# Performance work log

Measured on AMD Instinct MI355X. Metric: run time of the kernel, lower is better.

The kernel has to match this reference:

```python
import jax, jax.numpy as jnp
import numpy as np

B_SZ, L, D_MODEL = 4, 4096, 512
D_INNER, N_HEADS, HEAD_DIM = 1024, 16, 64
D_STATE, D_CONV, CHUNK = 64, 4, 64
EPS = 1e-5


def setup_inputs() -> dict:
    key = jax.random.key(0)
    ks = jax.random.split(key, 12)
    return {
        'x': jax.random.normal(ks[0], (B_SZ, L, D_MODEL), jnp.float32),
        'W_in': jax.random.normal(ks[1], (D_MODEL, 2 * D_INNER), jnp.float32) * 0.02,
        'conv_x_kernel': jax.random.normal(ks[2], (D_CONV, 1, D_INNER), jnp.float32) * 0.1,
        'conv_x_bias': jnp.zeros((D_INNER,), jnp.float32),
        'conv_z_kernel': jax.random.normal(ks[3], (D_CONV, 1, D_INNER), jnp.float32) * 0.1,
        'conv_z_bias': jnp.zeros((D_INNER,), jnp.float32),
        'W_xdbl': jax.random.normal(ks[4], (D_INNER, N_HEADS + 2 * D_STATE), jnp.float32) * 0.02,
        'dt_bias': jax.random.normal(ks[5], (N_HEADS,), jnp.float32) * 0.5,
        'A_log': jax.random.uniform(ks[6], (N_HEADS,), jnp.float32, 0.0, 1.0),
        'D': jnp.ones((N_HEADS,), jnp.float32),
        'norm_weight': jnp.ones((D_INNER,), jnp.float32),
        'W_out': jax.random.normal(ks[7], (D_INNER, D_MODEL), jnp.float32) * 0.02,
    }


def dwconv(x, kernel, bias):
    # x: (b, l, d); kernel: (k, 1, d) depthwise, flax 'SAME' padding
    out = jax.lax.conv_general_dilated(
        x, kernel, window_strides=(1,), padding='SAME',
        dimension_numbers=('NWC', 'WIO', 'NWC'),
        feature_group_count=x.shape[-1])
    return out + bias


def segsum(a):
    # stable segment-sum: out[..., d, e] = sum_{e < i <= d} a[..., i]; -inf above diag
    T = a.shape[-1]
    a_rep = jnp.broadcast_to(a[..., :, None], a.shape + (T,))
    strict = jnp.tril(jnp.ones((T, T), bool), -1)
    seg = jnp.cumsum(jnp.where(strict, a_rep, 0.0), axis=-2)
    return jnp.where(jnp.tril(jnp.ones((T, T), bool)), seg, -jnp.inf)


def ssd(x, A, B, C, chunk):
    # x: (b,l,h,p), A: (b,l,h), B/C: (b,l,n) (single group, broadcast over heads)
    b, l, h, p = x.shape
    c = l // chunk
    x = x.reshape(b, c, chunk, h, p)
    A = A.reshape(b, c, chunk, h).transpose(0, 3, 1, 2)  # (b,h,c,l)
    B = B.reshape(b, c, chunk, -1)
    C = C.reshape(b, c, chunk, -1)
    A_cum = jnp.cumsum(A, axis=-1)
    Lmat = jnp.exp(segsum(A))  # (b,h,c,l,l)
    Y_diag = jnp.einsum('bcln,bcsn,bhcls,bcshp->bclhp', C, B, Lmat, x)
    decay_states = jnp.exp(A_cum[..., -1:] - A_cum)
    states = jnp.einsum('bcln,bhcl,bclhp->bchpn', B, decay_states, x)
    states = jnp.concatenate([jnp.zeros_like(states[:, :1]), states], axis=1)
    A_last = jnp.pad(A_cum[..., -1], ((0, 0), (0, 0), (1, 0)))
    decay_chunk = jnp.exp(segsum(A_last))  # (b,h,c+1,c+1)
    new_states = jnp.einsum('bhzc,bchpn->bzhpn', decay_chunk, states)
    states, final_state = new_states[:, :-1], new_states[:, -1]
    Y_off = jnp.einsum('bcln,bchpn,bhcl->bclhp', C, states, jnp.exp(A_cum))
    Y = (Y_diag + Y_off).reshape(b, l, h, p)
    return Y, final_state


def reference(x, W_in, conv_x_kernel, conv_x_bias, conv_z_kernel, conv_z_bias,
              W_xdbl, dt_bias, A_log, D, norm_weight, W_out):
    b, l, _ = x.shape
    xz = x @ W_in
    xi, z = jnp.split(xz, 2, axis=-1)
    xi = jax.nn.silu(dwconv(xi, conv_x_kernel, conv_x_bias))
    z = jax.nn.silu(dwconv(z, conv_z_kernel, conv_z_bias))
    x_dbl = xi @ W_xdbl  # (b,l,h+2n)
    dt = x_dbl[..., :N_HEADS]
    Bmat = x_dbl[..., N_HEADS:N_HEADS + D_STATE]
    Cmat = x_dbl[..., N_HEADS + D_STATE:]
    dt = jax.nn.softplus(dt + dt_bias)  # (b,l,h)
    A = -jnp.exp(A_log)  # (h,)
    xh = xi.reshape(b, l, N_HEADS, HEAD_DIM)
    y, _ = ssd(xh * dt[..., None], A * dt, Bmat, Cmat, CHUNK)
    y = y + xh * D[..., None]
    y = y.reshape(b, l, D_INNER)
    # gated RMSNorm (Mamba2 style): gate with silu(z), then rmsnorm with weight
    y = y * jax.nn.silu(z)
    y = y * jax.lax.rsqrt(jnp.mean(y * y, axis=-1, keepdims=True) + EPS) * norm_weight
    return y @ W_out
```

## Files before the change

kernel.cpp:

```cpp
#include <hip/hip_runtime.h>
#include <hip/hip_bf16.h>
#include <cstdint>

#define B_SZn 4
#define SEQ_L 4096
#define D_MODELn 512
#define D_INNERn 1024
#define N_HEADSn 16
#define HEAD_DIMn 64
#define D_STATEn 64
#define CHUNKn 64
#define NCHUNK (SEQ_L / CHUNKn)
#define BL (B_SZn * SEQ_L)
#define XDBL_N (N_HEADSn + 2 * D_STATEn)

typedef __hip_bfloat16 bf16;
typedef __bf16 bf16x8 __attribute__((ext_vector_type(8)));
typedef float f32x4 __attribute__((ext_vector_type(4)));

__device__ __forceinline__ float silu_f(float v) {
    return v / (1.0f + expf(-v));
}
__device__ __forceinline__ float b2f(unsigned short u) {
    return __uint_as_float((unsigned)u << 16);
}
__device__ __forceinline__ unsigned short f2b(float f) {
    bf16 h = __float2bfloat16(f);
    return *(unsigned short*)&h;
}
__device__ __forceinline__ void stf(float* p, float v) { *p = v; }
__device__ __forceinline__ void stf(bf16* p, float v) { *p = __float2bfloat16(v); }

__device__ __forceinline__ float4 us4_to_f4(ushort4 u) {
    float4 f;
    f.x = b2f(u.x); f.y = b2f(u.y); f.z = b2f(u.z); f.w = b2f(u.w);
    return f;
}

__device__ __forceinline__ void async_copy16(void* lds, const void* g) {
    __builtin_amdgcn_global_load_lds(
        (const __attribute__((address_space(1))) unsigned int*)g,
        (__attribute__((address_space(3))) unsigned int*)lds, 16, 0, 0);
}

__global__ __launch_bounds__(256) void cvt_f32_bf16(
    const float* __restrict__ in, bf16* __restrict__ out) {
    const int idx = blockIdx.x * 256 + threadIdx.x;
    float4 v = *(const float4*)(in + (size_t)idx * 4);
    ushort4 o;
    o.x = f2b(v.x); o.y = f2b(v.y); o.z = f2b(v.z); o.w = f2b(v.w);
    *(ushort4*)((unsigned short*)out + (size_t)idx * 4) = o;
}

__global__ __launch_bounds__(256) void transpose_cvt(
    const float* __restrict__ in, bf16* __restrict__ out, int R, int C) {
    __shared__ float t[32][33];
    const int bc = blockIdx.x * 32, br = blockIdx.y * 32;
    const int tx = threadIdx.x & 31, ty = threadIdx.x >> 5;
#pragma unroll
    for (int i = ty; i < 32; i += 8) {
        int r = br + i, c = bc + tx;
        t[i][tx] = (r < R && c < C) ? in[(size_t)r * C + c] : 0.f;
    }
    __syncthreads();
#pragma unroll
    for (int i = ty; i < 32; i += 8) {
        int c = bc + i, r = br + tx;
        if (c < C && r < R) out[(size_t)c * R + r] = __float2bfloat16(t[tx][i]);
    }
}

template <typename TO>
__global__ __launch_bounds__(256) void gemm_mfma(
    const bf16* __restrict__ A, const bf16* __restrict__ Bt,
    TO* __restrict__ C, int M, int N, int K) {
    __shared__ __align__(16) unsigned short Al[2][128 * 32];
    __shared__ __align__(16) unsigned short Bl[2][128 * 32];
    const int tid = threadIdx.x;
    const int wave = tid >> 6, lane = tid & 63;
    const int wm = (wave >> 1) * 64, wn = (wave & 1) * 64;
    int lin = blockIdx.y * gridDim.x + blockIdx.x;
    const int nwg = gridDim.x * gridDim.y;
    if ((nwg & 7) == 0) lin = (lin & 7) * (nwg >> 3) + (lin >> 3);
    const int bm = (lin / gridDim.x) * 128, bn = (lin % gridDim.x) * 128;
    f32x4 acc[4][4];
#pragma unroll
    for (int m = 0; m < 4; ++m)
#pragma unroll
        for (int n = 0; n < 4; ++n) acc[m][n] = (f32x4)(0.f);

    const int lrow = lane & 15, lk8 = (lane >> 4) * 8;
    const int srow = tid >> 2, sc8 = (tid & 3) * 8;
    for (int k0 = 0; k0 < K; k0 += 64) {
#pragma unroll
        for (int h = 0; h < 2; ++h) {
            const int kh = k0 + h * 32;
            async_copy16((char*)&Al[h][0] + (size_t)(wave * 64) * 16,
                         A + (size_t)(bm + srow) * K + kh + sc8);
            async_copy16((char*)&Al[h][0] + (size_t)(256 + wave * 64) * 16,
                         A + (size_t)(bm + 64 + srow) * K + kh + sc8);
            async_copy16((char*)&Bl[h][0] + (size_t)(wave * 64) * 16,
                         Bt + (size_t)(bn + srow) * K + kh + sc8);
            async_copy16((char*)&Bl[h][0] + (size_t)(256 + wave * 64) * 16,
                         Bt + (size_t)(bn + 64 + srow) * K + kh + sc8);
        }
        __syncthreads();
#pragma unroll
        for (int h = 0; h < 2; ++h) {
            bf16x8 af[4], bfr[4];
#pragma unroll
            for (int m = 0; m < 4; ++m)
                af[m] = *(const bf16x8*)(&Al[h][(wm + m * 16 + lrow) * 32 + lk8]);
#pragma unroll
            for (int n = 0; n < 4; ++n)
                bfr[n] = *(const bf16x8*)(&Bl[h][(wn + n * 16 + lrow) * 32 + lk8]);
#pragma unroll
            for (int m = 0; m < 4; ++m)
#pragma unroll
                for (int n = 0; n < 4; ++n)
                    acc[m][n] = __builtin_amdgcn_mfma_f32_16x16x32_bf16(
                        af[m], bfr[n], acc[m][n], 0, 0, 0);
        }
        __syncthreads();
    }
#pragma unroll
    for (int m = 0; m < 4; ++m) {
#pragma unroll
        for (int n = 0; n < 4; ++n) {
#pragma unroll
            for (int r = 0; r < 4; ++r) {
                int row = bm + wm + m * 16 + (lane >> 4) * 4 + r;
                int col = bn + wn + n * 16 + (lane & 15);
                if (row < M && col < N)
                    stf(&C[(size_t)row * N + col], acc[m][n][r]);
            }
        }
    }
}

__global__ __launch_bounds__(256) void conv_silu_kernel(
    const bf16* __restrict__ xz,
    const float* __restrict__ kx, const float* __restrict__ bx,
    const float* __restrict__ kz, const float* __restrict__ bz,
    bf16* __restrict__ xi, bf16* __restrict__ zo) {
    const int tid = threadIdx.x;
    const int d4 = tid * 4;
    const int blk = blockIdx.x;
    const int l0 = (blk * 8) & (SEQ_L - 1);
    const int b = (blk * 8) >> 12;
    const unsigned short* base = (const unsigned short*)xz +
                                 ((size_t)b * SEQ_L) * (2 * D_INNERn);
    float4 wx[4], wz[4];
#pragma unroll
    for (int k = 0; k < 4; ++k) {
        wx[k] = *(const float4*)(kx + k * D_INNERn + d4);
        wz[k] = *(const float4*)(kz + k * D_INNERn + d4);
    }
    const float4 bxv = *(const float4*)(bx + d4);
    const float4 bzv = *(const float4*)(bz + d4);
    float4 vx[4], vz[4];
#pragma unroll
    for (int j = 0; j < 3; ++j) {
        int l = l0 - 1 + j;
        if (l >= 0) {
            const unsigned short* row = base + (size_t)l * (2 * D_INNERn);
            vx[j] = us4_to_f4(*(const ushort4*)(row + d4));
            vz[j] = us4_to_f4(*(const ushort4*)(row + D_INNERn + d4));
        } else {
            vx[j] = make_float4(0.f, 0.f, 0.f, 0.f);
            vz[j] = make_float4(0.f, 0.f, 0.f, 0.f);
        }
    }
    unsigned short* xout = (unsigned short*)xi;
    unsigned short* zout = (unsigned short*)zo;
#pragma unroll
    for (int j = 0; j < 8; ++j) {
        const int lread = l0 + 2 + j;
        if (lread < SEQ_L) {
            const unsigned short* row = base + (size_t)lread * (2 * D_INNERn);
            vx[3] = us4_to_f4(*(const ushort4*)(row + d4));
            vz[3] = us4_to_f4(*(const ushort4*)(row + D_INNERn + d4));
        } else {
            vx[3] = make_float4(0.f, 0.f, 0.f, 0.f);
            vz[3] = make_float4(0.f, 0.f, 0.f, 0.f);
        }
        float4 ax = bxv, az = bzv;
#pragma unroll
        for (int k = 0; k < 4; ++k) {
            ax.x += vx[k].x * wx[k].x; ax.y += vx[k].y * wx[k].y;
            ax.z += vx[k].z * wx[k].z; ax.w += vx[k].w * wx[k].w;
            az.x += vz[k].x * wz[k].x; az.y += vz[k].y * wz[k].y;
            az.z += vz[k].z * wz[k].z; az.w += vz[k].w * wz[k].w;
        }
        ushort4 ox, oz;
        ox.x = f2b(silu_f(ax.x)); ox.y = f2b(silu_f(ax.y));
        ox.z = f2b(silu_f(ax.z)); ox.w = f2b(silu_f(ax.w));
        oz.x = f2b(silu_f(az.x)); oz.y = f2b(silu_f(az.y));
        oz.z = f2b(silu_f(az.z)); oz.w = f2b(silu_f(az.w));
        const size_t obase = ((size_t)b * SEQ_L + l0 + j) * D_INNERn + d4;
        *(ushort4*)(xout + obase) = ox;
        *(ushort4*)(zout + obase) = oz;
        vx[0] = vx[1]; vx[1] = vx[2]; vx[2] = vx[3];
        vz[0] = vz[1]; vz[1] = vz[2]; vz[2] = vz[3];
    }
}

__global__ __launch_bounds__(256) void dt_kernel(
    const unsigned short* __restrict__ xdbl, const float* __restrict__ dt_bias,
    float* __restrict__ dtp) {
    const int idx = blockIdx.x * 256 + threadIdx.x;
    const int h = idx & 15;
    const int r = idx >> 4;
    float v = b2f(xdbl[(size_t)r * XDBL_N + h]) + dt_bias[h];
    dtp[idx] = (v > 20.f) ? v : log1pf(expf(v));
}

__global__ __launch_bounds__(256) void ssd_chunk_mfma(
    const unsigned short* __restrict__ xdbl, const bf16* __restrict__ xi,
    const float* __restrict__ dtp, const float* __restrict__ A_log,
    const float* __restrict__ Dvec,
    unsigned short* __restrict__ y, unsigned short* __restrict__ S,
    float* __restrict__ acum_g, float* __restrict__ rchunk) {
    __shared__ __align__(16) unsigned short sBb[64 * 72];
    __shared__ __align__(16) unsigned short sCb[64 * 72];
    __shared__ __align__(16) unsigned short sXT[64 * 72];
    __shared__ __align__(16) unsigned short sGb[64 * 72];
    __shared__ __align__(16) unsigned short sWB[64 * 72];
    __shared__ float sdtp[64], sacum[64], sw[64];
    const int bid = blockIdx.x;
    const int h = bid & 15;
    const int bc = bid >> 4;
    const int c = bc & (NCHUNK - 1);
    const int b = bc >> 6;
    const int tid = threadIdx.x;
    const int wave = tid >> 6, lane = tid & 63;
    const int lrow = lane & 15, lk8 = (lane >> 4) * 8;
    const int row0 = b * SEQ_L + c * CHUNKn;
    const float Ah = -expf(A_log[h]);
    const float Dh = Dvec[h];

    if (tid < 64) sdtp[tid] = dtp[(size_t)(row0 + tid) * N_HEADSn + h];
    const unsigned short* xius = (const unsigned short*)xi;
#pragma unroll
    for (int it = 0; it < 16; ++it) {
        int e = tid + it * 256;
        int s = e >> 6, n = e & 63;
        const unsigned short* xr = xdbl + (size_t)(row0 + s) * XDBL_N + N_HEADSn;
        sBb[s * 72 + n] = xr[n];
        sCb[s * 72 + n] = xr[D_STATEn + n];
        sXT[n * 72 + s] = xius[(size_t)(row0 + s) * D_INNERn + h * HEAD_DIMn + n];
    }
    __syncthreads();
    if (wave == 0) {
        float v = Ah * sdtp[lane];
#pragma unroll
        for (int o = 1; o < 64; o <<= 1) {
            float t = __shfl_up(v, o);
            if (lane >= o) v += t;
        }
        sacum[lane] = v;
        float last = __shfl(v, 63);
        sw[lane] = expf(last - v) * sdtp[lane];
        acum_g[(size_t)bid * 64 + lane] = v;
        if (lane == 63) rchunk[bid] = expf(v);
    }
    f32x4 acc1[4];
#pragma unroll
    for (int t = 0; t < 4; ++t) acc1[t] = (f32x4)(0.f);
#pragma unroll
    for (int ks = 0; ks < 2; ++ks) {
        bf16x8 a = *(const bf16x8*)(&sCb[(wave * 16 + lrow) * 72 + ks * 32 + lk8]);
#pragma unroll
        for (int t = 0; t < 4; ++t) {
            bf16x8 bb = *(const bf16x8*)(&sBb[(t * 16 + lrow) * 72 + ks * 32 + lk8]);
            acc1[t] = __builtin_amdgcn_mfma_f32_16x16x32_bf16(a, bb, acc1[t], 0, 0, 0);
        }
    }
    __syncthreads();
#pragma unroll
    for (int t = 0; t < 4; ++t) {
#pragma unroll
        for (int r = 0; r < 4; ++r) {
            int l = wave * 16 + (lane >> 4) * 4 + r;
            int s = t * 16 + lrow;
            float val = 0.f;
            if (l >= s) val = acc1[t][r] * expf(sacum[l] - sacum[s]) * sdtp[s];
            sGb[l * 72 + s] = f2b(val);
        }
    }
#pragma unroll
    for (int it = 0; it < 16; ++it) {
        int e = tid + it * 256;
        int s = e >> 6, n = e & 63;
        sWB[n * 72 + s] = f2b(sw[s] * b2f(sBb[s * 72 + n]));
    }
    __syncthreads();
    f32x4 acc2[4], acc3[4];
#pragma unroll
    for (int t = 0; t < 4; ++t) { acc2[t] = (f32x4)(0.f); acc3[t] = (f32x4)(0.f); }
#pragma unroll
    for (int ks = 0; ks < 2; ++ks) {
        bf16x8 a2 = *(const bf16x8*)(&sGb[(wave * 16 + lrow) * 72 + ks * 32 + lk8]);
        bf16x8 a3 = *(const bf16x8*)(&sXT[(wave * 16 + lrow) * 72 + ks * 32 + lk8]);
#pragma unroll
        for (int t = 0; t < 4; ++t) {
            bf16x8 b2v = *(const bf16x8*)(&sXT[(t * 16 + lrow) * 72 + ks * 32 + lk8]);
            bf16x8 b3v = *(const bf16x8*)(&sWB[(t * 16 + lrow) * 72 + ks * 32 + lk8]);
            acc2[t] = __builtin_amdgcn_mfma_f32_16x16x32_bf16(a2, b2v, acc2[t], 0, 0, 0);
            acc3[t] = __builtin_amdgcn_mfma_f32_16x16x32_bf16(a3, b3v, acc3[t], 0, 0, 0);
        }
    }
#pragma unroll
    for (int t = 0; t < 4; ++t) {
#pragma unroll
        for (int r = 0; r < 4; ++r) {
            int rr = wave * 16 + (lane >> 4) * 4 + r;
            int cc = t * 16 + lrow;
            float xv = b2f(sXT[cc * 72 + rr]);
            y[(size_t)(row0 + rr) * D_INNERn + h * HEAD_DIMn + cc] =
                f2b(acc2[t][r] + Dh * xv);
            S[(size_t)bid * 4096 + rr * 64 + cc] = f2b(acc3[t][r]);
        }
    }
}

__global__ __launch_bounds__(256) void chunk_scan_kernel(
    unsigned short* __restrict__ S, const float* __restrict__ rchunk) {
    const int idx = blockIdx.x * 256 + threadIdx.x;
    const int pn2 = (idx & 2047) * 2;
    const int bh = idx >> 11;
    const int h = bh & 15;
    const int b = bh >> 4;
    float P0 = 0.f, P1 = 0.f;
    for (int c = 0; c < NCHUNK; ++c) {
        int bid = (b * NCHUNK + c) * N_HEADSn + h;
        size_t off = (size_t)bid * 4096 + pn2;
        unsigned int v = *(unsigned int*)(S + off);
        float s0 = b2f((unsigned short)(v & 0xffff));
        float s1 = b2f((unsigned short)(v >> 16));
        *(unsigned int*)(S + off) =
            (unsigned int)f2b(P0) | ((unsigned int)f2b(P1) << 16);
        float rc = rchunk[bid];
        P0 = rc * P0 + s0;
        P1 = rc * P1 + s1;
    }
}

__global__ __launch_bounds__(256) void yoff_mfma(
    const unsigned short* __restrict__ xdbl, const unsigned short* __restrict__ S,
    const float* __restrict__ acum_g, unsigned short* __restrict__ y) {
    __shared__ __align__(16) unsigned short sCb[64 * 72];
    __shared__ __align__(16) unsigned short sP[64 * 72];
    __shared__ float se[64];
    const int bid = blockIdx.x;
    const int h = bid & 15;
    const int bc = bid >> 4;
    const int c = bc & (NCHUNK - 1);
    const int b = bc >> 6;
    const int tid = threadIdx.x;
    const int wave = tid >> 6, lane = tid & 63;
    const int lrow = lane & 15, lk8 = (lane >> 4) * 8;
    const int row0 = b * SEQ_L + c * CHUNKn;
    if (tid < 64) se[tid] = expf(acum_g[(size_t)bid * 64 + tid]);
#pragma unroll
    for (int it = 0; it < 16; ++it) {
        int e = tid + it * 256;
        int r = e >> 6, n = e & 63;
        sCb[r * 72 + n] = xdbl[(size_t)(row0 + r) * XDBL_N + N_HEADSn + D_STATEn + n];
        sP[r * 72 + n] = S[(size_t)bid * 4096 + e];
    }
    __syncthreads();
    f32x4 acc[4];
#pragma unroll
    for (int t = 0; t < 4; ++t) acc[t] = (f32x4)(0.f);
#pragma unroll
    for (int ks = 0; ks < 2; ++ks) {
        bf16x8 a = *(const bf16x8*)(&sCb[(wave * 16 + lrow) * 72 + ks * 32 + lk8]);
#pragma unroll
        for (int t = 0; t < 4; ++t) {
            bf16x8 bb = *(const bf16x8*)(&sP[(t * 16 + lrow) * 72 + ks * 32 + lk8]);
            acc[t] = __builtin_amdgcn_mfma_f32_16x16x32_bf16(a, bb, acc[t], 0, 0, 0);
        }
    }
#pragma unroll
    for (int t = 0; t < 4; ++t) {
#pragma unroll
        for (int r = 0; r < 4; ++r) {
            int l = wave * 16 + (lane >> 4) * 4 + r;
            int p = t * 16 + lrow;
            size_t idx = (size_t)(row0 + l) * D_INNERn + h * HEAD_DIMn + p;
            y[idx] = f2b(b2f(y[idx]) + acc[t][r] * se[l]);
        }
    }
}

__global__ __launch_bounds__(256) void gate_norm_kernel(
    const unsigned short* __restrict__ y, const bf16* __restrict__ zb,
    const float* __restrict__ nw, bf16* __restrict__ y_bf) {
    const int row = blockIdx.x;
    const int tid = threadIdx.x;
    const size_t base = (size_t)row * D_INNERn + tid * 4;
    ushort4 yu = *(const ushort4*)(y + base);
    ushort4 zu = *(const ushort4*)((const unsigned short*)zb + base);
    float v0 = b2f(yu.x) * silu_f(b2f(zu.x));
    float v1 = b2f(yu.y) * silu_f(b2f(zu.y));
    float v2 = b2f(yu.z) * silu_f(b2f(zu.z));
    float v3 = b2f(yu.w) * silu_f(b2f(zu.w));
    float ss = v0 * v0 + v1 * v1 + v2 * v2 + v3 * v3;
#pragma unroll
    for (int o = 32; o > 0; o >>= 1) ss += __shfl_xor(ss, o);
    __shared__ float sred[4];
    if ((tid & 63) == 0) sred[tid >> 6] = ss;
    __syncthreads();
    float total = sred[0] + sred[1] + sred[2] + sred[3];
    float scale = rsqrtf(total * (1.0f / D_INNERn) + 1e-5f);
    float4 wv = *(const float4*)(nw + tid * 4);
    ushort4 o4;
    o4.x = f2b(v0 * scale * wv.x);
    o4.y = f2b(v1 * scale * wv.y);
    o4.z = f2b(v2 * scale * wv.z);
    o4.w = f2b(v3 * scale * wv.w);
    *(ushort4*)((unsigned short*)y_bf + base) = o4;
}

extern "C" void kernel_launch(void* const* d_in, const int* in_sizes, int n_in,
                              void* d_out, int out_size, void* d_ws, size_t ws_size,
                              hipStream_t stream) {
    (void)in_sizes; (void)n_in; (void)out_size; (void)ws_size;
    const float* x       = (const float*)d_in[0];
    const float* W_in    = (const float*)d_in[1];
    const float* ckx     = (const float*)d_in[2];
    const float* cbx     = (const float*)d_in[3];
    const float* ckz     = (const float*)d_in[4];
    const float* cbz     = (const float*)d_in[5];
    const float* W_xdbl  = (const float*)d_in[6];
    const float* dt_bias = (const float*)d_in[7];
    const float* A_log   = (const float*)d_in[8];
    const float* Dvec    = (const float*)d_in[9];
    const float* nw      = (const float*)d_in[10];
    const float* W_out   = (const float*)d_in[11];
    float* out = (float*)d_out;
    char* w = (char*)d_ws;

    bf16*  xz     = (bf16*)(w);
    unsigned short* y = (unsigned short*)(w);
    bf16*  xi     = (bf16*)(w + 67108864);
    bf16*  zb     = (bf16*)(w + 100663296);
    char*  Sreg   = w + 134217728;
    unsigned short* S = (unsigned short*)Sreg;
    bf16*  x_bf   = (bf16*)Sreg;
    bf16*  W_in_T = (bf16*)(Sreg + 16777216);
    bf16*  W_xd_T = (bf16*)(Sreg + 18874368);
    bf16*  y_bf   = (bf16*)Sreg;
    bf16*  W_o_T  = (bf16*)(Sreg + 33554432);
    unsigned short* xdbl = (unsigned short*)(w + 201326592);
    float* dtp    = (float*)(w + 210763776);
    float* acum   = (float*)(w + 211812352);
    float* rchunk = (float*)(w + 212860928);

    cvt_f32_bf16<<<BL * D_MODELn / 1024, 256, 0, stream>>>(x, x_bf);
    transpose_cvt<<<dim3(2048 / 32, 512 / 32), 256, 0, stream>>>(W_in, W_in_T, 512, 2048);
    transpose_cvt<<<dim3(5, 1024 / 32), 256, 0, stream>>>(W_xdbl, W_xd_T, 1024, 144);
    gemm_mfma<bf16><<<dim3(2048 / 128, BL / 128), 256, 0, stream>>>(
        x_bf, W_in_T, xz, BL, 2048, D_MODELn);
    conv_silu_kernel<<<BL / 8, 256, 0, stream>>>(xz, ckx, cbx, ckz, cbz, xi, zb);
    gemm_mfma<bf16><<<dim3(2, BL / 128), 256, 0, stream>>>(
        xi, W_xd_T, (bf16*)xdbl, BL, XDBL_N, D_INNERn);
    dt_kernel<<<BL * N_HEADSn / 256, 256, 0, stream>>>(xdbl, dt_bias, dtp);
    ssd_chunk_mfma<<<B_SZn * NCHUNK * N_HEADSn, 256, 0, stream>>>(
        xdbl, xi, dtp, A_log, Dvec, y, S, acum, rchunk);
    chunk_scan_kernel<<<B_SZn * N_HEADSn * 2048 / 256, 256, 0, stream>>>(S, rchunk);
    yoff_mfma<<<B_SZn * NCHUNK * N_HEADSn, 256, 0, stream>>>(xdbl, S, acum, y);
    transpose_cvt<<<dim3(512 / 32, 1024 / 32), 256, 0, stream>>>(W_out, W_o_T, 1024, 512);
    gate_norm_kernel<<<BL, 256, 0, stream>>>(y, zb, nw, y_bf);
    gemm_mfma<float><<<dim3(512 / 128, BL / 128), 256, 0, stream>>>(
        y_bf, W_o_T, out, BL, D_MODELn, D_INNERn);
}
```

Before: 257.8 us.

## Double-buffer GEMM K-loop and fuse softplus dt into SSD chunk kernel

The GEMM main loop now prefetches the next 32-wide K slice into the alternate LDS buffer while MFMAs run on the current one, replacing the load-all-then-compute pattern with two barriers per 64-K step. Separately, the standalone dt_kernel is removed and the softplus of dt plus bias is computed inline in ssd_chunk_mfma, eliminating a launch and an intermediate buffer round-trip. The pipelined loop trades one barrier per 32-K step and relies on async copies landing before the end-of-iteration sync. The fused softplus is recomputed per head-chunk block, a small amount of redundant work.

Result: no change. 261.5 us (+1.4%).

```diff
diff --git a/kernel.cpp b/kernel.cpp
--- a/kernel.cpp
+++ b/kernel.cpp
@@ -91,37 +91,36 @@
 
     const int lrow = lane & 15, lk8 = (lane >> 4) * 8;
     const int srow = tid >> 2, sc8 = (tid & 3) * 8;
-    for (int k0 = 0; k0 < K; k0 += 64) {
-#pragma unroll
-        for (int h = 0; h < 2; ++h) {
-            const int kh = k0 + h * 32;
-            async_copy16((char*)&Al[h][0] + (size_t)(wave * 64) * 16,
-                         A + (size_t)(bm + srow) * K + kh + sc8);
-            async_copy16((char*)&Al[h][0] + (size_t)(256 + wave * 64) * 16,
-                         A + (size_t)(bm + 64 + srow) * K + kh + sc8);
-            async_copy16((char*)&Bl[h][0] + (size_t)(wave * 64) * 16,
-                         Bt + (size_t)(bn + srow) * K + kh + sc8);
-            async_copy16((char*)&Bl[h][0] + (size_t)(256 + wave * 64) * 16,
-                         Bt + (size_t)(bn + 64 + srow) * K + kh + sc8);
-        }
+    auto STAGE = [&](int buf, int k) {
+        async_copy16((char*)&Al[buf][0] + (size_t)(wave * 64) * 16,
+                     A + (size_t)(bm + srow) * K + k + sc8);
+        async_copy16((char*)&Al[buf][0] + (size_t)(256 + wave * 64) * 16,
+                     A + (size_t)(bm + 64 + srow) * K + k + sc8);
+        async_copy16((char*)&Bl[buf][0] + (size_t)(wave * 64) * 16,
+                     Bt + (size_t)(bn + srow) * K + k + sc8);
+        async_copy16((char*)&Bl[buf][0] + (size_t)(256 + wave * 64) * 16,
+                     Bt + (size_t)(bn + 64 + srow) * K + k + sc8);
+    };
+    STAGE(0, 0);
+    __syncthreads();
+    int cur = 0;
+    for (int k0 = 0; k0 < K; k0 += 32) {
+        if (k0 + 32 < K) STAGE(cur ^ 1, k0 + 32);
+        bf16x8 af[4], bfr[4];
+#pragma unroll
+        for (int m = 0; m < 4; ++m)
+            af[m] = *(const bf16x8*)(&Al[cur][(wm + m * 16 + lrow) * 32 + lk8]);
+#pragma unroll
+        for (int n = 0; n < 4; ++n)
+            bfr[n] = *(const bf16x8*)(&Bl[cur][(wn + n * 16 + lrow) * 32 + lk8]);
+#pragma unroll
+        for (int m = 0; m < 4; ++m)
+#pragma unroll
+            for (int n = 0; n < 4; ++n)
+                acc[m][n] = __builtin_amdgcn_mfma_f32_16x16x32_bf16(
+                    af[m], bfr[n], acc[m][n], 0, 0, 0);
         __syncthreads();
-#pragma unroll
-        for (int h = 0; h < 2; ++h) {
-            bf16x8 af[4], bfr[4];
-#pragma unroll
-            for (int m = 0; m < 4; ++m)
-                af[m] = *(const bf16x8*)(&Al[h][(wm + m * 16 + lrow) * 32 + lk8]);
-#pragma unroll
-            for (int n = 0; n < 4; ++n)
-                bfr[n] = *(const bf16x8*)(&Bl[h][(wn + n * 16 + lrow) * 32 + lk8]);
-#pragma unroll
-            for (int m = 0; m < 4; ++m)
-#pragma unroll
-                for (int n = 0; n < 4; ++n)
-                    acc[m][n] = __builtin_amdgcn_mfma_f32_16x16x32_bf16(
-                        af[m], bfr[n], acc[m][n], 0, 0, 0);
-        }
-        __syncthreads();
+        cur ^= 1;
     }
 #pragma unroll
     for (int m = 0; m < 4; ++m) {
@@ -205,19 +204,9 @@
     }
 }
 
-__global__ __launch_bounds__(256) void dt_kernel(
-    const unsigned short* __restrict__ xdbl, const float* __restrict__ dt_bias,
-    float* __restrict__ dtp) {
-    const int idx = blockIdx.x * 256 + threadIdx.x;
-    const int h = idx & 15;
-    const int r = idx >> 4;
-    float v = b2f(xdbl[(size_t)r * XDBL_N + h]) + dt_bias[h];
-    dtp[idx] = (v > 20.f) ? v : log1pf(expf(v));
-}
-
 __global__ __launch_bounds__(256) void ssd_chunk_mfma(
     const unsigned short* __restrict__ xdbl, const bf16* __restrict__ xi,
-    const float* __restrict__ dtp, const float* __restrict__ A_log,
+    const float* __restrict__ dt_bias, const float* __restrict__ A_log,
     const float* __restrict__ Dvec,
     unsigned short* __restrict__ y, unsigned short* __restrict__ S,
     float* __restrict__ acum_g, float* __restrict__ rchunk) {
@@ -239,7 +228,10 @@
     const float Ah = -expf(A_log[h]);
     const float Dh = Dvec[h];
 
-    if (tid < 64) sdtp[tid] = dtp[(size_t)(row0 + tid) * N_HEADSn + h];
+    if (tid < 64) {
+        float v = b2f(xdbl[(size_t)(row0 + tid) * XDBL_N + h]) + dt_bias[h];
+        sdtp[tid] = (v > 20.f) ? v : log1pf(expf(v));
+    }
     const unsigned short* xius = (const unsigned short*)xi;
 #pragma unroll
     for (int it = 0; it < 16; ++it) {
@@ -454,7 +446,6 @@
     bf16*  y_bf   = (bf16*)Sreg;
     bf16*  W_o_T  = (bf16*)(Sreg + 33554432);
     unsigned short* xdbl = (unsigned short*)(w + 201326592);
-    float* dtp    = (float*)(w + 210763776);
     float* acum   = (float*)(w + 211812352);
     float* rchunk = (float*)(w + 212860928);
 
@@ -466,9 +457,8 @@
     conv_silu_kernel<<<BL / 8, 256, 0, stream>>>(xz, ckx, cbx, ckz, cbz, xi, zb);
     gemm_mfma<bf16><<<dim3(2, BL / 128), 256, 0, stream>>>(
         xi, W_xd_T, (bf16*)xdbl, BL, XDBL_N, D_INNERn);
-    dt_kernel<<<BL * N_HEADSn / 256, 256, 0, stream>>>(xdbl, dt_bias, dtp);
     ssd_chunk_mfma<<<B_SZn * NCHUNK * N_HEADSn, 256, 0, stream>>>(
-        xdbl, xi, dtp, A_log, Dvec, y, S, acum, rchunk);
+        xdbl, xi, dt_bias, A_log, Dvec, y, S, acum, rchunk);
     chunk_scan_kernel<<<B_SZn * N_HEADSn * 2048 / 256, 256, 0, stream>>>(S, rchunk);
     yoff_mfma<<<B_SZn * NCHUNK * N_HEADSn, 256, 0, stream>>>(xdbl, S, acum, y);
     transpose_cvt<<<dim3(512 / 32, 1024 / 32), 256, 0, stream>>>(W_out, W_o_T, 1024, 512);
```
